# Kernel optimization log

Measured on AMD Instinct MI355X. Metric: run time of the kernel, lower is better.

## Reference

```python
import jax, jax.numpy as jnp
import numpy as np

B, S, H, NH = 4, 1024, 2048, 16
D = H // NH  # head_dim = 128


def setup_inputs() -> dict:
    key = jax.random.key(0)
    ks = jax.random.split(key, 10)
    # RoPE tables: angle[t, j] = t * 10000^(-2j/D), cos/sin of the complex freqs_cis
    t = jnp.arange(S, dtype=jnp.float32)
    inv_freq = 1.0 / (10000.0 ** (jnp.arange(0, D, 2, dtype=jnp.float32) / D))
    ang = t[:, None] * inv_freq[None, :]  # [S, D//2]
    w = 0.02
    return {
        "hidden_states": jax.random.normal(ks[0], (B, S, H), jnp.float32),
        "freqs_cos": jnp.cos(ang),
        "freqs_sin": jnp.sin(ang),
        "attention_mask": jnp.ones((B, 1, 1, S), jnp.float32),
        "Wq": jax.random.normal(ks[1], (H, H), jnp.float32) * w,
        "bq": jnp.zeros((H,), jnp.float32),
        "Wk": jax.random.normal(ks[2], (H, H), jnp.float32) * w,
        "bk": jnp.zeros((H,), jnp.float32),
        "Wv": jax.random.normal(ks[3], (H, H), jnp.float32) * w,
        "bv": jnp.zeros((H,), jnp.float32),
        "Wo": jax.random.normal(ks[4], (H, H), jnp.float32) * w,
        "bo": jnp.zeros((H,), jnp.float32),
    }


def _rope(x, cos, sin):
    # x: [B, S, NH, D]; cos/sin: [S, D//2]. Complex multiply on (even, odd) pairs.
    x2 = x.reshape(x.shape[:-1] + (D // 2, 2))
    x0, x1 = x2[..., 0], x2[..., 1]
    c = cos[None, :, None, :]
    s = sin[None, :, None, :]
    o0 = x0 * c - x1 * s
    o1 = x0 * s + x1 * c
    return jnp.stack([o0, o1], axis=-1).reshape(x.shape)


def reference(hidden_states, freqs_cos, freqs_sin, attention_mask,
              Wq, bq, Wk, bk, Wv, bv, Wo, bo):
    b, s, _ = hidden_states.shape
    q = (hidden_states @ Wq.T + bq).reshape(b, s, NH, D)
    k = (hidden_states @ Wk.T + bk).reshape(b, s, NH, D)
    v = (hidden_states @ Wv.T + bv).reshape(b, s, NH, D)
    q = _rope(q, freqs_cos, freqs_sin)
    k = _rope(k, freqs_cos, freqs_sin)
    # scores: [b, h, q, k]; original scales by sqrt(embed_dim)=sqrt(hidden_size)
    scores = jnp.einsum('bqhd,bkhd->bhqk', q, k) / jnp.sqrt(jnp.float32(H))
    scores = jnp.where(attention_mask == 0, jnp.float32(-1e9), scores)
    probs = jax.nn.softmax(scores, axis=-1)  # dropout is identity in eval
    ctx = jnp.einsum('bhqk,bkhd->bqhd', probs, v).reshape(b, s, H)
    return ctx @ Wo.T + bo
```

## Files before the change

kernel.cpp:

```cpp
#include <hip/hip_runtime.h>
#include <stdint.h>

#define BATCH 4
#define SEQ   1024
#define NHEAD 16
#define DHEAD 128
#define HDIM  2048
#define GM    4096
#define GN    2048
#define GK    2048

typedef __attribute__((ext_vector_type(8))) short short8;
typedef __attribute__((ext_vector_type(4))) float f32x4;

__device__ __forceinline__ uint16_t f2bf(float f) {
  uint32_t u = __builtin_bit_cast(uint32_t, f);
  u += 0x7fffu + ((u >> 16) & 1u);
  return (uint16_t)(u >> 16);
}
__device__ __forceinline__ float bf2f(uint16_t h) {
  return __builtin_bit_cast(float, (uint32_t)h << 16);
}

__device__ __forceinline__ uint32_t swz64(uint32_t a)  { return a ^ (((a >> 7) & 3u) << 4); }
__device__ __forceinline__ uint32_t swz128(uint32_t a) { return a ^ (((a >> 7) & 7u) << 4); }
__device__ __forceinline__ uint32_t swz256(uint32_t a) { return a ^ (((a >> 8) & 7u) << 4); }

#define GAS __attribute__((address_space(1)))
#define LAS __attribute__((address_space(3)))
__device__ __forceinline__ void gload_lds16(const void* g, void* l) {
  __builtin_amdgcn_global_load_lds((GAS const void*)g, (LAS void*)l, 16, 0, 0);
}

__global__ void cvt_kernel(const float* __restrict__ in, uint16_t* __restrict__ out, int n8) {
  int i = blockIdx.x * 256 + threadIdx.x;
  if (i >= n8) return;
  const float4* p = (const float4*)in + (size_t)i * 2;
  float4 a = p[0], b = p[1];
  uint32_t w0 = f2bf(a.x) | ((uint32_t)f2bf(a.y) << 16);
  uint32_t w1 = f2bf(a.z) | ((uint32_t)f2bf(a.w) << 16);
  uint32_t w2 = f2bf(b.x) | ((uint32_t)f2bf(b.y) << 16);
  uint32_t w3 = f2bf(b.z) | ((uint32_t)f2bf(b.w) << 16);
  int4 r; r.x = (int)w0; r.y = (int)w1; r.z = (int)w2; r.w = (int)w3;
  *(int4*)(out + (size_t)i * 8) = r;
}

__global__ void cvtw_kernel(const float* __restrict__ W0, const float* __restrict__ W1,
                            const float* __restrict__ W2, const float* __restrict__ W3,
                            uint16_t* __restrict__ out) {
  const float* src = (blockIdx.y == 0) ? W0 : (blockIdx.y == 1) ? W1 : (blockIdx.y == 2) ? W2 : W3;
  int i = blockIdx.x * 256 + threadIdx.x;
  const float4* p = (const float4*)src + (size_t)i * 2;
  float4 a = p[0], b = p[1];
  uint32_t w0 = f2bf(a.x) | ((uint32_t)f2bf(a.y) << 16);
  uint32_t w1 = f2bf(a.z) | ((uint32_t)f2bf(a.w) << 16);
  uint32_t w2 = f2bf(b.x) | ((uint32_t)f2bf(b.y) << 16);
  uint32_t w3 = f2bf(b.z) | ((uint32_t)f2bf(b.w) << 16);
  int4 r; r.x = (int)w0; r.y = (int)w1; r.z = (int)w2; r.w = (int)w3;
  *(int4*)(out + (size_t)blockIdx.y * HDIM * HDIM + (size_t)i * 8) = r;
}

template <int MODE>
__device__ __forceinline__ void gemm_body(const uint16_t* __restrict__ A,
                                          const uint16_t* __restrict__ Bw,
                                          const float* __restrict__ bias,
                                          const float* __restrict__ fcos,
                                          const float* __restrict__ fsin,
                                          bool dorope,
                                          void* __restrict__ Cout) {
  __shared__ __align__(16) char smA[128 * 64];
  __shared__ __align__(16) char smB[128 * 64];
  const int tid = threadIdx.x, lane = tid & 63, wid = tid >> 6;
  const int c = lane & 15, g = lane >> 4;
  const int row0 = blockIdx.x * 128, col0 = blockIdx.y * 128;
  const int wr = wid >> 1, wc = wid & 1;
  f32x4 acc[4][4] = {};
  const uint32_t oBase = wid * 2048 + lane * 16;

  for (int kk = 0; kk < GK; kk += 32) {
#pragma unroll
    for (int q = 0; q < 2; ++q) {
      uint32_t o = oBase + q * 1024;
      uint32_t r = o >> 6;
      uint32_t cb = swz64(o) & 63;
      gload_lds16((const char*)A + ((size_t)(row0 + r) * GK + kk) * 2 + cb,
                  smA + wid * 2048 + q * 1024);
      gload_lds16((const char*)Bw + ((size_t)(col0 + r) * GK + kk) * 2 + cb,
                  smB + wid * 2048 + q * 1024);
    }
    __syncthreads();
    short8 af[4], bf[4];
#pragma unroll
    for (int m = 0; m < 4; ++m)
      af[m] = *(const short8*)(smA + swz64((uint32_t)((wr * 64 + m * 16 + c) * 64 + g * 16)));
#pragma unroll
    for (int n = 0; n < 4; ++n)
      bf[n] = *(const short8*)(smB + swz64((uint32_t)((wc * 64 + n * 16 + c) * 64 + g * 16)));
#pragma unroll
    for (int m = 0; m < 4; ++m)
#pragma unroll
      for (int n = 0; n < 4; ++n)
        acc[m][n] = __builtin_amdgcn_mfma_f32_16x16x32_bf16(af[m], bf[n], acc[m][n], 0, 0, 0);
    __syncthreads();
  }

  float bn[4];
#pragma unroll
  for (int n = 0; n < 4; ++n) bn[n] = bias[col0 + wc * 64 + n * 16 + c];
#pragma unroll
  for (int m = 0; m < 4; ++m) {
#pragma unroll
    for (int jj = 0; jj < 4; ++jj) {
      const int row = row0 + wr * 64 + m * 16 + g * 4 + jj;
      const int s = row & (SEQ - 1);
#pragma unroll
      for (int n = 0; n < 4; ++n) {
        const int d = wc * 64 + n * 16 + c;
        float v = acc[m][n][jj] + bn[n];
        float res = v;
        if (dorope) {
          float cs = fcos[s * 64 + (d >> 1)];
          float sn = fsin[s * 64 + (d >> 1)];
          float o = __shfl_xor(v, 1, 64);
          res = (c & 1) ? (o * sn + v * cs) : (v * cs - o * sn);
        }
        const size_t idx = (size_t)row * GN + col0 + d;
        if (MODE == 1) ((float*)Cout)[idx] = res;
        else           ((uint16_t*)Cout)[idx] = f2bf(res);
      }
    }
  }
}

__global__ __launch_bounds__(256, 2) void gemm_qkv_kernel(
    const uint16_t* __restrict__ X,
    const uint16_t* __restrict__ Wq, const uint16_t* __restrict__ Wk, const uint16_t* __restrict__ Wv,
    const float* __restrict__ bq, const float* __restrict__ bk, const float* __restrict__ bv,
    const float* __restrict__ fcos, const float* __restrict__ fsin,
    uint16_t* __restrict__ qo, uint16_t* __restrict__ ko, uint16_t* __restrict__ vo) {
  const uint16_t* W; const float* bias; uint16_t* out;
  if (blockIdx.z == 0)      { W = Wq; bias = bq; out = qo; }
  else if (blockIdx.z == 1) { W = Wk; bias = bk; out = ko; }
  else                      { W = Wv; bias = bv; out = vo; }
  gemm_body<0>(X, W, bias, fcos, fsin, blockIdx.z < 2, out);
}

__global__ __launch_bounds__(256, 2) void gemm_out_kernel(
    const uint16_t* __restrict__ ctx, const uint16_t* __restrict__ Wo,
    const float* __restrict__ bo, float* __restrict__ out) {
  gemm_body<1>(ctx, Wo, bo, nullptr, nullptr, false, out);
}

__global__ __launch_bounds__(256, 2) void attn_kernel(
    const uint16_t* __restrict__ q, const uint16_t* __restrict__ k,
    const uint16_t* __restrict__ v, const float* __restrict__ mask,
    uint16_t* __restrict__ ctx) {
  __shared__ __align__(16) char smK[64 * 256];
  __shared__ __align__(16) char smVT[128 * 128];
  __shared__ __align__(16) char smP[64 * 128];
  __shared__ float smMask[64];
  __shared__ float smScale[64];

  const int tid = threadIdx.x, lane = tid & 63, wid = tid >> 6;
  const int c = lane & 15, g = lane >> 4;
  const int b = blockIdx.z, h = blockIdx.y, q0 = blockIdx.x * 64;
  const float scale = 0.022097086912079608f;

  short8 qreg[4];
  {
    const uint16_t* qrow = q + (size_t)(b * SEQ + q0 + wid * 16 + c) * HDIM + h * DHEAD;
#pragma unroll
    for (int ks = 0; ks < 4; ++ks) qreg[ks] = *(const short8*)(qrow + ks * 32 + g * 8);
  }

  const int kvg = tid >> 5;
  const int d0  = (tid & 31) * 4;

  float mreg = -1e30f, lreg = 0.f;
  f32x4 oacc[8] = {};

  for (int t = 0; t < 16; ++t) {
    const int kv0 = t * 64;
    __syncthreads();
#pragma unroll
    for (int i = 0; i < 4; ++i) {
      uint32_t o = wid * 4096 + i * 1024 + lane * 16;
      uint32_t r = o >> 8;
      uint32_t cb = swz256(o) & 255;
      gload_lds16((const char*)k + ((size_t)(b * SEQ + kv0 + r) * HDIM + h * DHEAD) * 2 + cb,
                  smK + wid * 4096 + i * 1024);
    }
    if (tid < 64) smMask[tid] = mask[b * SEQ + kv0 + tid];
    {
      const uint16_t* vsrc = v + (size_t)(b * SEQ + kv0 + kvg * 8) * HDIM + h * DHEAD + d0;
      uint32_t vw[8][2];
#pragma unroll
      for (int e = 0; e < 8; ++e) {
        uint2 t2 = *(const uint2*)(vsrc + (size_t)e * HDIM);
        vw[e][0] = t2.x; vw[e][1] = t2.y;
      }
#pragma unroll
      for (int j = 0; j < 4; ++j) {
        const int hw = j >> 1, sh = (j & 1) * 16;
        int4 pk;
        pk.x = (int)(((vw[0][hw] >> sh) & 0xffffu) | (((vw[1][hw] >> sh) & 0xffffu) << 16));
        pk.y = (int)(((vw[2][hw] >> sh) & 0xffffu) | (((vw[3][hw] >> sh) & 0xffffu) << 16));
        pk.z = (int)(((vw[4][hw] >> sh) & 0xffffu) | (((vw[5][hw] >> sh) & 0xffffu) << 16));
        pk.w = (int)(((vw[6][hw] >> sh) & 0xffffu) | (((vw[7][hw] >> sh) & 0xffffu) << 16));
        *(int4*)(smVT + swz128((uint32_t)((d0 + j) * 128 + kvg * 16))) = pk;
      }
    }
    __syncthreads();

    f32x4 st[4] = {};
#pragma unroll
    for (int ks = 0; ks < 4; ++ks) {
#pragma unroll
      for (int mi = 0; mi < 4; ++mi) {
        short8 kf = *(const short8*)(smK + swz256((uint32_t)((mi * 16 + c) * 256 + ks * 64 + g * 16)));
        st[mi] = __builtin_amdgcn_mfma_f32_16x16x32_bf16(kf, qreg[ks], st[mi], 0, 0, 0);
      }
    }
    float sv[4][4];
    float pmax = -1e30f;
#pragma unroll
    for (int mi = 0; mi < 4; ++mi) {
      float4 mb = *(const float4*)(smMask + mi * 16 + g * 4);
      float mbv[4] = {mb.x, mb.y, mb.z, mb.w};
#pragma unroll
      for (int jj = 0; jj < 4; ++jj) {
        float s = st[mi][jj] * scale;
        if (mbv[jj] == 0.f) s = -1e9f;
        sv[mi][jj] = s;
        pmax = fmaxf(pmax, s);
      }
    }
    pmax = fmaxf(pmax, __shfl_xor(pmax, 16, 64));
    pmax = fmaxf(pmax, __shfl_xor(pmax, 32, 64));
    float mnew = fmaxf(mreg, pmax);
    float fac = __expf(mreg - mnew);
    float rsum = 0.f;
    uint32_t pw[4][2];
#pragma unroll
    for (int mi = 0; mi < 4; ++mi) {
      float p0 = __expf(sv[mi][0] - mnew);
      float p1 = __expf(sv[mi][1] - mnew);
      float p2 = __expf(sv[mi][2] - mnew);
      float p3 = __expf(sv[mi][3] - mnew);
      rsum += (p0 + p1) + (p2 + p3);
      pw[mi][0] = f2bf(p0) | ((uint32_t)f2bf(p1) << 16);
      pw[mi][1] = f2bf(p2) | ((uint32_t)f2bf(p3) << 16);
    }
    rsum += __shfl_xor(rsum, 16, 64);
    rsum += __shfl_xor(rsum, 32, 64);
    lreg = lreg * fac + rsum;
    mreg = mnew;
#pragma unroll
    for (int mi = 0; mi < 4; ++mi) {
      uint32_t addr = swz128((uint32_t)((wid * 16 + c) * 128 + (mi * 16 + g * 4) * 2));
      uint2 wv; wv.x = pw[mi][0]; wv.y = pw[mi][1];
      *(uint2*)(smP + addr) = wv;
    }
    if (g == 0) smScale[wid * 16 + c] = fac;
    __syncthreads();

    float4 fv = *(const float4*)(smScale + wid * 16 + g * 4);
    float fvv[4] = {fv.x, fv.y, fv.z, fv.w};
#pragma unroll
    for (int nj = 0; nj < 8; ++nj)
#pragma unroll
      for (int jj = 0; jj < 4; ++jj) oacc[nj][jj] *= fvv[jj];
#pragma unroll
    for (int ks = 0; ks < 2; ++ks) {
      short8 pf = *(const short8*)(smP + swz128((uint32_t)((wid * 16 + c) * 128 + ks * 64 + g * 16)));
#pragma unroll
      for (int nj = 0; nj < 8; ++nj) {
        short8 vf = *(const short8*)(smVT + swz128((uint32_t)((nj * 16 + c) * 128 + ks * 64 + g * 16)));
        oacc[nj] = __builtin_amdgcn_mfma_f32_16x16x32_bf16(pf, vf, oacc[nj], 0, 0, 0);
      }
    }
  }

  __syncthreads();
  if (g == 0) smScale[wid * 16 + c] = lreg;
  __syncthreads();
  float4 lv = *(const float4*)(smScale + wid * 16 + g * 4);
  float inv[4] = {1.f / lv.x, 1.f / lv.y, 1.f / lv.z, 1.f / lv.w};
#pragma unroll
  for (int nj = 0; nj < 8; ++nj) {
#pragma unroll
    for (int jj = 0; jj < 4; ++jj) {
      int qrow = q0 + wid * 16 + g * 4 + jj;
      int dcol = h * DHEAD + nj * 16 + c;
      ctx[(size_t)(b * SEQ + qrow) * HDIM + dcol] = f2bf(oacc[nj][jj] * inv[jj]);
    }
  }
}

extern "C" void kernel_launch(void* const* d_in, const int* in_sizes, int n_in,
                              void* d_out, int out_size, void* d_ws, size_t ws_size,
                              hipStream_t stream) {
  const float* hs   = (const float*)d_in[0];
  const float* fcos = (const float*)d_in[1];
  const float* fsin = (const float*)d_in[2];
  const float* mask = (const float*)d_in[3];
  const float* Wq = (const float*)d_in[4];  const float* bq = (const float*)d_in[5];
  const float* Wk = (const float*)d_in[6];  const float* bk = (const float*)d_in[7];
  const float* Wv = (const float*)d_in[8];  const float* bv = (const float*)d_in[9];
  const float* Wo = (const float*)d_in[10]; const float* bo = (const float*)d_in[11];
  float* out = (float*)d_out;

  char* ws = (char*)d_ws;
  const size_t XB = (size_t)GM * HDIM * 2;
  const size_t WB = (size_t)HDIM * HDIM * 2;
  uint16_t* Xbf = (uint16_t*)(ws);
  uint16_t* Wqb = (uint16_t*)(ws + XB);
  uint16_t* Wkb = (uint16_t*)(ws + XB + WB);
  uint16_t* Wvb = (uint16_t*)(ws + XB + 2 * WB);
  uint16_t* Wob = (uint16_t*)(ws + XB + 3 * WB);
  uint16_t* qb  = (uint16_t*)(ws + XB + 4 * WB);
  uint16_t* kb  = (uint16_t*)(ws + XB + 4 * WB + XB);
  uint16_t* vb  = (uint16_t*)(ws + XB + 4 * WB + 2 * XB);

  cvt_kernel<<<4096, 256, 0, stream>>>(hs, Xbf, (GM * HDIM) / 8);
  cvtw_kernel<<<dim3(2048, 4), 256, 0, stream>>>(Wq, Wk, Wv, Wo, Wqb);

  gemm_qkv_kernel<<<dim3(GM / 128, GN / 128, 3), 256, 0, stream>>>(
      Xbf, Wqb, Wkb, Wvb, bq, bk, bv, fcos, fsin, qb, kb, vb);

  attn_kernel<<<dim3(SEQ / 64, NHEAD, BATCH), 256, 0, stream>>>(qb, kb, vb, mask, Xbf);

  gemm_out_kernel<<<dim3(GM / 128, GN / 128, 1), 256, 0, stream>>>(Xbf, Wob, bo, out);
}
```

Before: 292.5 us.

## Double GEMM K-step to 64 and move RoPE into a separate elementwise kernel

The shared GEMM body now stages 64-wide K slices (128-byte rows with an XOR swizzle) instead of 32-wide ones. This halves the number of barrier pairs and loop iterations and issues twice as many MFMAs per sync. The RoPE rotation is removed from the GEMM epilogue, which had per-element cos/sin loads and shuffles, and is done by a new vectorised kernel that reads and rewrites q and k in place. The cost is doubled LDS per block, which may reduce occupancy, plus one extra kernel launch and an extra read and write pass over q and k.

```diff
diff --git a/kernel.cpp b/kernel.cpp
--- a/kernel.cpp
+++ b/kernel.cpp
@@ -22,7 +22,6 @@
   return __builtin_bit_cast(float, (uint32_t)h << 16);
 }
 
-__device__ __forceinline__ uint32_t swz64(uint32_t a)  { return a ^ (((a >> 7) & 3u) << 4); }
 __device__ __forceinline__ uint32_t swz128(uint32_t a) { return a ^ (((a >> 7) & 7u) << 4); }
 __device__ __forceinline__ uint32_t swz256(uint32_t a) { return a ^ (((a >> 8) & 7u) << 4); }
 
@@ -60,47 +59,78 @@
   *(int4*)(out + (size_t)blockIdx.y * HDIM * HDIM + (size_t)i * 8) = r;
 }
 
+__global__ void rope_kernel(uint16_t* __restrict__ qb, uint16_t* __restrict__ kb,
+                            const float* __restrict__ fcos, const float* __restrict__ fsin) {
+  uint32_t i = blockIdx.x * 256 + threadIdx.x;
+  uint16_t* p = (blockIdx.y == 0 ? qb : kb) + (size_t)i * 8;
+  uint32_t e0 = i * 8;
+  uint32_t row = e0 >> 11;
+  uint32_t col = e0 & 2047;
+  uint32_t s = row & (SEQ - 1);
+  uint32_t pi = (col & (DHEAD - 1)) >> 1;
+  float4 cv = *(const float4*)(fcos + (size_t)s * 64 + pi);
+  float4 sv = *(const float4*)(fsin + (size_t)s * 64 + pi);
+  int4 raw = *(const int4*)p;
+  uint16_t u[8]; *(int4*)u = raw;
+  float cc[4] = {cv.x, cv.y, cv.z, cv.w}, ss[4] = {sv.x, sv.y, sv.z, sv.w};
+#pragma unroll
+  for (int t = 0; t < 4; ++t) {
+    float x0 = bf2f(u[2 * t]), x1 = bf2f(u[2 * t + 1]);
+    float o0 = x0 * cc[t] - x1 * ss[t];
+    float o1 = x0 * ss[t] + x1 * cc[t];
+    u[2 * t] = f2bf(o0); u[2 * t + 1] = f2bf(o1);
+  }
+  *(int4*)p = *(int4*)u;
+}
+
 template <int MODE>
 __device__ __forceinline__ void gemm_body(const uint16_t* __restrict__ A,
                                           const uint16_t* __restrict__ Bw,
                                           const float* __restrict__ bias,
-                                          const float* __restrict__ fcos,
-                                          const float* __restrict__ fsin,
-                                          bool dorope,
                                           void* __restrict__ Cout) {
-  __shared__ __align__(16) char smA[128 * 64];
-  __shared__ __align__(16) char smB[128 * 64];
+  __shared__ __align__(16) char smA[128 * 128];
+  __shared__ __align__(16) char smB[128 * 128];
   const int tid = threadIdx.x, lane = tid & 63, wid = tid >> 6;
   const int c = lane & 15, g = lane >> 4;
   const int row0 = blockIdx.x * 128, col0 = blockIdx.y * 128;
   const int wr = wid >> 1, wc = wid & 1;
   f32x4 acc[4][4] = {};
-  const uint32_t oBase = wid * 2048 + lane * 16;
-
-  for (int kk = 0; kk < GK; kk += 32) {
-#pragma unroll
-    for (int q = 0; q < 2; ++q) {
+  const uint32_t oBase = wid * 4096 + lane * 16;
+
+  for (int kk = 0; kk < GK; kk += 64) {
+#pragma unroll
+    for (int q = 0; q < 4; ++q) {
       uint32_t o = oBase + q * 1024;
-      uint32_t r = o >> 6;
-      uint32_t cb = swz64(o) & 63;
+      uint32_t r = o >> 7;
+      uint32_t cb = (o & 127) ^ ((r & 7u) << 4);
       gload_lds16((const char*)A + ((size_t)(row0 + r) * GK + kk) * 2 + cb,
-                  smA + wid * 2048 + q * 1024);
+                  smA + wid * 4096 + q * 1024);
       gload_lds16((const char*)Bw + ((size_t)(col0 + r) * GK + kk) * 2 + cb,
-                  smB + wid * 2048 + q * 1024);
-    }
-    __syncthreads();
-    short8 af[4], bf[4];
+                  smB + wid * 4096 + q * 1024);
+    }
+    __syncthreads();
+    short8 af[4][2], bf[4][2];
+#pragma unroll
+    for (int m = 0; m < 4; ++m) {
+      const uint32_t row = (uint32_t)(wr * 64 + m * 16 + c);
+#pragma unroll
+      for (int ks = 0; ks < 2; ++ks)
+        af[m][ks] = *(const short8*)(smA + row * 128 + (((uint32_t)(ks * 64 + g * 16)) ^ ((row & 7u) << 4)));
+    }
+#pragma unroll
+    for (int n = 0; n < 4; ++n) {
+      const uint32_t row = (uint32_t)(wc * 64 + n * 16 + c);
+#pragma unroll
+      for (int ks = 0; ks < 2; ++ks)
+        bf[n][ks] = *(const short8*)(smB + row * 128 + (((uint32_t)(ks * 64 + g * 16)) ^ ((row & 7u) << 4)));
+    }
 #pragma unroll
     for (int m = 0; m < 4; ++m)
-      af[m] = *(const short8*)(smA + swz64((uint32_t)((wr * 64 + m * 16 + c) * 64 + g * 16)));
-#pragma unroll
-    for (int n = 0; n < 4; ++n)
-      bf[n] = *(const short8*)(smB + swz64((uint32_t)((wc * 64 + n * 16 + c) * 64 + g * 16)));
-#pragma unroll
-    for (int m = 0; m < 4; ++m)
 #pragma unroll
       for (int n = 0; n < 4; ++n)
-        acc[m][n] = __builtin_amdgcn_mfma_f32_16x16x32_bf16(af[m], bf[n], acc[m][n], 0, 0, 0);
+#pragma unroll
+        for (int ks = 0; ks < 2; ++ks)
+          acc[m][n] = __builtin_amdgcn_mfma_f32_16x16x32_bf16(af[m][ks], bf[n][ks], acc[m][n], 0, 0, 0);
     __syncthreads();
   }
 
@@ -109,24 +139,15 @@
   for (int n = 0; n < 4; ++n) bn[n] = bias[col0 + wc * 64 + n * 16 + c];
 #pragma unroll
   for (int m = 0; m < 4; ++m) {
-#pragma unroll
-    for (int jj = 0; jj < 4; ++jj) {
-      const int row = row0 + wr * 64 + m * 16 + g * 4 + jj;
-      const int s = row & (SEQ - 1);
-#pragma unroll
-      for (int n = 0; n < 4; ++n) {
-        const int d = wc * 64 + n * 16 + c;
+    const int gr = row0 + wr * 64 + m * 16 + g * 4;
+#pragma unroll
+    for (int n = 0; n < 4; ++n) {
+      const int gc = col0 + wc * 64 + n * 16 + c;
+#pragma unroll
+      for (int jj = 0; jj < 4; ++jj) {
         float v = acc[m][n][jj] + bn[n];
-        float res = v;
-        if (dorope) {
-          float cs = fcos[s * 64 + (d >> 1)];
-          float sn = fsin[s * 64 + (d >> 1)];
-          float o = __shfl_xor(v, 1, 64);
-          res = (c & 1) ? (o * sn + v * cs) : (v * cs - o * sn);
-        }
-        const size_t idx = (size_t)row * GN + col0 + d;
-        if (MODE == 1) ((float*)Cout)[idx] = res;
-        else           ((uint16_t*)Cout)[idx] = f2bf(res);
+        if (MODE == 1) ((float*)Cout)[(size_t)(gr + jj) * GN + gc] = v;
+        else           ((uint16_t*)Cout)[(size_t)(gr + jj) * GN + gc] = f2bf(v);
       }
     }
   }
@@ -136,19 +157,18 @@
     const uint16_t* __restrict__ X,
     const uint16_t* __restrict__ Wq, const uint16_t* __restrict__ Wk, const uint16_t* __restrict__ Wv,
     const float* __restrict__ bq, const float* __restrict__ bk, const float* __restrict__ bv,
-    const float* __restrict__ fcos, const float* __restrict__ fsin,
     uint16_t* __restrict__ qo, uint16_t* __restrict__ ko, uint16_t* __restrict__ vo) {
   const uint16_t* W; const float* bias; uint16_t* out;
   if (blockIdx.z == 0)      { W = Wq; bias = bq; out = qo; }
   else if (blockIdx.z == 1) { W = Wk; bias = bk; out = ko; }
   else                      { W = Wv; bias = bv; out = vo; }
-  gemm_body<0>(X, W, bias, fcos, fsin, blockIdx.z < 2, out);
+  gemm_body<0>(X, W, bias, out);
 }
 
 __global__ __launch_bounds__(256, 2) void gemm_out_kernel(
     const uint16_t* __restrict__ ctx, const uint16_t* __restrict__ Wo,
     const float* __restrict__ bo, float* __restrict__ out) {
-  gemm_body<1>(ctx, Wo, bo, nullptr, nullptr, false, out);
+  gemm_body<1>(ctx, Wo, bo, out);
 }
 
 __global__ __launch_bounds__(256, 2) void attn_kernel(
@@ -326,7 +346,9 @@
   cvtw_kernel<<<dim3(2048, 4), 256, 0, stream>>>(Wq, Wk, Wv, Wo, Wqb);
 
   gemm_qkv_kernel<<<dim3(GM / 128, GN / 128, 3), 256, 0, stream>>>(
-      Xbf, Wqb, Wkb, Wvb, bq, bk, bv, fcos, fsin, qb, kb, vb);
+      Xbf, Wqb, Wkb, Wvb, bq, bk, bv, qb, kb, vb);
+
+  rope_kernel<<<dim3((GM * HDIM) / 8 / 256, 2, 1), 256, 0, stream>>>(qb, kb, fcos, fsin);
 
   attn_kernel<<<dim3(SEQ / 64, NHEAD, BATCH), 256, 0, stream>>>(qb, kb, vb, mask, Xbf);
 
```

New measurement: 280.0 us. -4.3%, faster.
